# Optimization experiments

Hardware: AMD Instinct MI355X
Metric: run time of the kernel (lower is better)

The kernel has to match this reference:

```python
import jax, jax.numpy as jnp
import numpy as np


def setup_inputs() -> dict:
    key = jax.random.key(0)
    k1, k2 = jax.random.split(key)
    B, N, M, D = 4, 4096, 4096, 32
    x1 = jax.random.normal(k1, (B, N, D), dtype=jnp.float32)
    x2 = jax.random.normal(k2, (B, M, D), dtype=jnp.float32)
    const = jnp.ones((1,), dtype=jnp.float32)
    return {"x1": x1, "x2": x2, "const": const}


def reference(x1, x2, const):
    # Pairwise dot products: [B,N,D] x [B,M,D] -> [B,N,M], then add scalar bias.
    # (Original materializes an O(N*M*D) broadcast intermediate; einsum/bmm avoids it.)
    numerator = jnp.einsum("bnd,bmd->bnm", x1, x2)
    return numerator + const
```

## Files before the change

### kernel.cpp

```cpp
#include <hip/hip_runtime.h>


constexpr int Bv = 4;
constexpr int Nv = 4096;
constexpr int Mv = 4096;
constexpr int Dv = 32;
constexpr int TM = 128;
constexpr int TN = 128;
constexpr int LROW = 132;

__global__ __launch_bounds__(256, 2)
void pairwise_dot_bias_kernel(const float* __restrict__ x1,
                              const float* __restrict__ x2,
                              const float* __restrict__ cbias,
                              float* __restrict__ out) {
    __shared__ float a_s[Dv][LROW];
    __shared__ float b_s[Dv][LROW];

    const int b  = blockIdx.z;
    const int n0 = blockIdx.y * TM;
    const int m0 = blockIdx.x * TN;
    const int t  = threadIdx.x;

    const float* x1b = x1 + (size_t)b * Nv * Dv + (size_t)n0 * Dv;
    const float* x2b = x2 + (size_t)b * Mv * Dv + (size_t)m0 * Dv;

    #pragma unroll
    for (int p = 0; p < 4; ++p) {
        const int flat = p * 1024 + t * 4;
        const int row  = flat >> 5;
        const int col  = flat & 31;
        const float4 av = *reinterpret_cast<const float4*>(x1b + flat);
        const float4 bv = *reinterpret_cast<const float4*>(x2b + flat);
        a_s[col + 0][row] = av.x;
        a_s[col + 1][row] = av.y;
        a_s[col + 2][row] = av.z;
        a_s[col + 3][row] = av.w;
        b_s[col + 0][row] = bv.x;
        b_s[col + 1][row] = bv.y;
        b_s[col + 2][row] = bv.z;
        b_s[col + 3][row] = bv.w;
    }
    __syncthreads();

    const int tx = t & 15;
    const int ty = t >> 4;

    float acc[8][8];
    #pragma unroll
    for (int i = 0; i < 8; ++i)
        #pragma unroll
        for (int j = 0; j < 8; ++j)
            acc[i][j] = 0.0f;

    #pragma unroll
    for (int d = 0; d < Dv; ++d) {
        const float4 a0 = *reinterpret_cast<const float4*>(&a_s[d][ty * 8]);
        const float4 a1 = *reinterpret_cast<const float4*>(&a_s[d][ty * 8 + 4]);
        const float4 b0 = *reinterpret_cast<const float4*>(&b_s[d][tx * 8]);
        const float4 b1 = *reinterpret_cast<const float4*>(&b_s[d][tx * 8 + 4]);
        const float av[8] = {a0.x, a0.y, a0.z, a0.w, a1.x, a1.y, a1.z, a1.w};
        const float bw[8] = {b0.x, b0.y, b0.z, b0.w, b1.x, b1.y, b1.z, b1.w};
        #pragma unroll
        for (int i = 0; i < 8; ++i)
            #pragma unroll
            for (int j = 0; j < 8; ++j)
                acc[i][j] = fmaf(av[i], bw[j], acc[i][j]);
    }

    const float cb = cbias[0];
    float* outb = out + (size_t)b * Nv * Mv;
    #pragma unroll
    for (int i = 0; i < 8; ++i) {
        float* orow = outb + (size_t)(n0 + ty * 8 + i) * Mv + (m0 + tx * 8);
        float4 v0, v1;
        v0.x = acc[i][0] + cb; v0.y = acc[i][1] + cb;
        v0.z = acc[i][2] + cb; v0.w = acc[i][3] + cb;
        v1.x = acc[i][4] + cb; v1.y = acc[i][5] + cb;
        v1.z = acc[i][6] + cb; v1.w = acc[i][7] + cb;
        *reinterpret_cast<float4*>(orow)     = v0;
        *reinterpret_cast<float4*>(orow + 4) = v1;
    }
}

extern "C" void kernel_launch(void* const* d_in, const int* in_sizes, int n_in,
                              void* d_out, int out_size, void* d_ws, size_t ws_size,
                              hipStream_t stream) {
    const float* x1 = (const float*)d_in[0];
    const float* x2 = (const float*)d_in[1];
    const float* cb = (const float*)d_in[2];
    float* out = (float*)d_out;

    dim3 grid(Mv / TN, Nv / TM, Bv);
    pairwise_dot_bias_kernel<<<grid, 256, 0, stream>>>(x1, x2, cb, out);
}
```

Baseline: 80.35 us.

## Compute pairwise dots with fp16 MFMA instructions loading fragments directly from global memory

```diff
diff --git a/kernel.cpp b/kernel.cpp
--- a/kernel.cpp
+++ b/kernel.cpp
@@ -1,85 +1,68 @@
 #include <hip/hip_runtime.h>
 
+
+typedef _Float16 half8 __attribute__((ext_vector_type(8)));
+typedef float    f32x4 __attribute__((ext_vector_type(4)));
 
 constexpr int Bv = 4;
 constexpr int Nv = 4096;
 constexpr int Mv = 4096;
 constexpr int Dv = 32;
 constexpr int TM = 128;
-constexpr int TN = 128;
-constexpr int LROW = 132;
+constexpr int TN = 256;
 
 __global__ __launch_bounds__(256, 2)
-void pairwise_dot_bias_kernel(const float* __restrict__ x1,
-                              const float* __restrict__ x2,
-                              const float* __restrict__ cbias,
-                              float* __restrict__ out) {
-    __shared__ float a_s[Dv][LROW];
-    __shared__ float b_s[Dv][LROW];
-
+void pairwise_dot_bias_mfma(const float* __restrict__ x1,
+                            const float* __restrict__ x2,
+                            const float* __restrict__ cbias,
+                            float* __restrict__ out) {
     const int b  = blockIdx.z;
     const int n0 = blockIdx.y * TM;
     const int m0 = blockIdx.x * TN;
     const int t  = threadIdx.x;
+    const int w    = t >> 6;
+    const int lane = t & 63;
+    const int l16  = lane & 15;
+    const int lh   = lane >> 4;
 
-    const float* x1b = x1 + (size_t)b * Nv * Dv + (size_t)n0 * Dv;
-    const float* x2b = x2 + (size_t)b * Mv * Dv + (size_t)m0 * Dv;
+    const float* x1b = x1 + (size_t)b * Nv * Dv;
+    const float* x2b = x2 + (size_t)b * Mv * Dv;
+    const float  cb  = cbias[0];
+    float* outb = out + (size_t)b * Nv * Mv;
+
+    half8 afrag[8];
+    #pragma unroll
+    for (int rg = 0; rg < 8; ++rg) {
+        const float* p = x1b + (size_t)(n0 + rg * 16 + l16) * Dv + lh * 8;
+        const f32x4 f0 = *reinterpret_cast<const f32x4*>(p);
+        const f32x4 f1 = *reinterpret_cast<const f32x4*>(p + 4);
+        afrag[rg][0] = (_Float16)f0.x; afrag[rg][1] = (_Float16)f0.y;
+        afrag[rg][2] = (_Float16)f0.z; afrag[rg][3] = (_Float16)f0.w;
+        afrag[rg][4] = (_Float16)f1.x; afrag[rg][5] = (_Float16)f1.y;
+        afrag[rg][6] = (_Float16)f1.z; afrag[rg][7] = (_Float16)f1.w;
+    }
 
     #pragma unroll
-    for (int p = 0; p < 4; ++p) {
-        const int flat = p * 1024 + t * 4;
-        const int row  = flat >> 5;
-        const int col  = flat & 31;
-        const float4 av = *reinterpret_cast<const float4*>(x1b + flat);
-        const float4 bv = *reinterpret_cast<const float4*>(x2b + flat);
-        a_s[col + 0][row] = av.x;
-        a_s[col + 1][row] = av.y;
-        a_s[col + 2][row] = av.z;
-        a_s[col + 3][row] = av.w;
-        b_s[col + 0][row] = bv.x;
-        b_s[col + 1][row] = bv.y;
-        b_s[col + 2][row] = bv.z;
-        b_s[col + 3][row] = bv.w;
-    }
-    __syncthreads();
+    for (int c = 0; c < 4; ++c) {
+        const int mcol = m0 + w * 64 + c * 16 + l16;
+        const float* p = x2b + (size_t)mcol * Dv + lh * 8;
+        const f32x4 g0 = *reinterpret_cast<const f32x4*>(p);
+        const f32x4 g1 = *reinterpret_cast<const f32x4*>(p + 4);
+        half8 bfrag;
+        bfrag[0] = (_Float16)g0.x; bfrag[1] = (_Float16)g0.y;
+        bfrag[2] = (_Float16)g0.z; bfrag[3] = (_Float16)g0.w;
+        bfrag[4] = (_Float16)g1.x; bfrag[5] = (_Float16)g1.y;
+        bfrag[6] = (_Float16)g1.z; bfrag[7] = (_Float16)g1.w;
 
-    const int tx = t & 15;
-    const int ty = t >> 4;
-
-    float acc[8][8];
-    #pragma unroll
-    for (int i = 0; i < 8; ++i)
         #pragma unroll
-        for (int j = 0; j < 8; ++j)
-            acc[i][j] = 0.0f;
-
-    #pragma unroll
-    for (int d = 0; d < Dv; ++d) {
-        const float4 a0 = *reinterpret_cast<const float4*>(&a_s[d][ty * 8]);
-        const float4 a1 = *reinterpret_cast<const float4*>(&a_s[d][ty * 8 + 4]);
-        const float4 b0 = *reinterpret_cast<const float4*>(&b_s[d][tx * 8]);
-        const float4 b1 = *reinterpret_cast<const float4*>(&b_s[d][tx * 8 + 4]);
-        const float av[8] = {a0.x, a0.y, a0.z, a0.w, a1.x, a1.y, a1.z, a1.w};
-        const float bw[8] = {b0.x, b0.y, b0.z, b0.w, b1.x, b1.y, b1.z, b1.w};
-        #pragma unroll
-        for (int i = 0; i < 8; ++i)
+        for (int rg = 0; rg < 8; ++rg) {
+            f32x4 acc = {0.f, 0.f, 0.f, 0.f};
+            acc = __builtin_amdgcn_mfma_f32_16x16x32_f16(afrag[rg], bfrag, acc, 0, 0, 0);
+            const int rbase = n0 + rg * 16 + lh * 4;
             #pragma unroll
-            for (int j = 0; j < 8; ++j)
-                acc[i][j] = fmaf(av[i], bw[j], acc[i][j]);
-    }
-
-    const float cb = cbias[0];
-    float* outb = out + (size_t)b * Nv * Mv;
-    #pragma unroll
-    for (int i = 0; i < 8; ++i) {
-        float* orow = outb + (size_t)(n0 + ty * 8 + i) * Mv + (m0 + tx * 8);
-        float4 v0, v1;
-        v0.x = acc[i][0] + cb; v0.y = acc[i][1] + cb;
-        v0.z = acc[i][2] + cb; v0.w = acc[i][3] + cb;
-        v1.x = acc[i][4] + cb; v1.y = acc[i][5] + cb;
-        v1.z = acc[i][6] + cb; v1.w = acc[i][7] + cb;
-        *reinterpret_cast<float4*>(orow)     = v0;
-        *reinterpret_cast<float4*>(orow + 4) = v1;
+            for (int r = 0; r < 4; ++r)
+                outb[(size_t)(rbase + r) * Mv + mcol] = acc[r] + cb;
+        }
     }
 }
 
@@ -92,5 +75,5 @@
     float* out = (float*)d_out;
 
     dim3 grid(Mv / TN, Nv / TM, Bv);
-    pairwise_dot_bias_kernel<<<grid, 256, 0, stream>>>(x1, x2, cb, out);
+    pairwise_dot_bias_mfma<<<grid, 256, 0, stream>>>(x1, x2, cb, out);
 }
```

New measurement: 68.88 us. 14.3% less time.
